# Kernel tuning notes

Hardware: AMD Instinct MI355X
Metric: run time of the kernel (lower is better)

The kernel has to match this reference:

```python
import jax, jax.numpy as jnp
import numpy as np

B, T, F, D = 4, 512, 512, 256


def setup_inputs() -> dict:
    key = jax.random.key(0)
    ks = jax.random.split(key, 7)
    x = jax.random.normal(ks[0], (B, T, F), jnp.float32)
    state = jnp.zeros((B, D, D), jnp.float32)
    init = lambda k, shape, fan: jax.random.normal(k, shape, jnp.float32) / np.sqrt(fan).astype(np.float32)
    Wk = init(ks[1], (F, D), F)
    Wq = init(ks[2], (F, D), F)
    Wv = init(ks[3], (F, D), F)
    Wbeta = init(ks[4], (F, 1), F)
    gamma = jnp.ones((F,), jnp.float32)
    beta_ln = jnp.zeros((F,), jnp.float32)
    Wsc = init(ks[5], (F, D), F)
    bsc = jnp.zeros((D,), jnp.float32)
    return dict(x=x, state=state, Wk=Wk, Wq=Wq, Wv=Wv, Wbeta=Wbeta,
                gamma=gamma, beta_ln=beta_ln, Wsc=Wsc, bsc=bsc)


def _layernorm(x, gamma, beta):
    mu = x.mean(-1, keepdims=True)
    var = x.var(-1, keepdims=True)  # ddof=0, matches torch LayerNorm
    return (x - mu) * jax.lax.rsqrt(var + 1e-5) * gamma + beta


def reference(x, state, Wk, Wq, Wv, Wbeta, gamma, beta_ln, Wsc, bsc):
    xn = _layernorm(x, gamma, beta_ln)                       # [B,T,F]
    K = jax.nn.relu(xn @ Wk)                                 # [B,T,D]
    Q = jax.nn.relu(xn @ Wq)                                 # [B,T,D]
    V = xn @ Wv                                              # [B,T,D]
    beta = jax.nn.sigmoid(xn @ Wbeta)                        # [B,T,1]
    # sum normalization
    K = K / (1e-5 + K.sum(-1, keepdims=True))
    Q = Q / (1e-5 + Q.sum(-1, keepdims=True))

    def step(s, inp):
        k, v, b = inp                                        # k,v:[B,D], b:[B,1]
        vbar = jnp.einsum('bij,bj->bi', s, k)                # retrieve
        s = s + (b * (v - vbar))[:, :, None] * k[:, None, :] # outer-product write
        return s, s

    Kt = jnp.moveaxis(K, 1, 0)  # [T,B,D]
    Vt = jnp.moveaxis(V, 1, 0)
    bt = jnp.moveaxis(beta, 1, 0)  # [T,B,1]
    _, states = jax.lax.scan(step, state, (Kt, Vt, bt))      # [T,B,D,D]
    states = jnp.moveaxis(states, 0, 1)                      # [B,T,D,D]

    y = jnp.einsum('btij,btj->bti', states, Q)               # [B,T,D]
    y = y + xn @ Wsc + bsc                                   # residual shortcut
    return y, states
```

## Files before the change

### kernel.cpp

```cpp
#include <hip/hip_runtime.h>
#include <math.h>

#define Bc 4
#define Tc 512
#define Fc 512
#define Dc 256
#define RPB 8
#define PF 4
#define CH 16
#define RS 4
#define NC (Tc / CH)

typedef float floatx4 __attribute__((ext_vector_type(4)));

__device__ __forceinline__ float wred(float v) {
#pragma unroll
  for (int off = 32; off; off >>= 1) v += __shfl_xor(v, off, 64);
  return v;
}

__device__ __forceinline__ float rl(float v, int l) {
  return __int_as_float(__builtin_amdgcn_readlane(__float_as_int(v), l));
}

__device__ __forceinline__ void wred2_dpp(float& a, float& c) {
#define DPP_STEP(ctrl, rmask)                                                 \
  {                                                                           \
    float ta = __int_as_float(__builtin_amdgcn_update_dpp(                    \
        0, __float_as_int(a), (ctrl), (rmask), 0xf, true));                   \
    float tc = __int_as_float(__builtin_amdgcn_update_dpp(                    \
        0, __float_as_int(c), (ctrl), (rmask), 0xf, true));                   \
    a += ta;                                                                  \
    c += tc;                                                                  \
  }
  DPP_STEP(0x111, 0xf)
  DPP_STEP(0x112, 0xf)
  DPP_STEP(0x114, 0xf)
  DPP_STEP(0x118, 0xf)
  DPP_STEP(0x142, 0xa)
  DPP_STEP(0x143, 0xc)
#undef DPP_STEP
  a = rl(a, 63);
  c = rl(c, 63);
}

__device__ __forceinline__ void ln_rows(const float* __restrict__ x,
                                        const float* __restrict__ gamma,
                                        const float* __restrict__ beta_ln,
                                        int row0, int wave, int lane,
                                        float (*xnL)[Fc]) {
#pragma unroll
  for (int rr = 0; rr < 2; ++rr) {
    const int r = wave * 2 + rr;
    const float* xr = x + (size_t)(row0 + r) * Fc;
    float4 a = *(const float4*)&xr[lane * 8];
    float4 b = *(const float4*)&xr[lane * 8 + 4];
    float s8 = a.x + a.y + a.z + a.w + b.x + b.y + b.z + b.w;
    float mu = wred(s8) * (1.0f / Fc);
    float d0 = a.x - mu, d1 = a.y - mu, d2 = a.z - mu, d3 = a.w - mu;
    float d4 = b.x - mu, d5 = b.y - mu, d6 = b.z - mu, d7 = b.w - mu;
    float sq = d0 * d0 + d1 * d1 + d2 * d2 + d3 * d3 + d4 * d4 + d5 * d5 +
               d6 * d6 + d7 * d7;
    float var = wred(sq) * (1.0f / Fc);
    float rs = rsqrtf(var + 1e-5f);
    float4 g0 = *(const float4*)&gamma[lane * 8];
    float4 g1 = *(const float4*)&gamma[lane * 8 + 4];
    float4 bl0 = *(const float4*)&beta_ln[lane * 8];
    float4 bl1 = *(const float4*)&beta_ln[lane * 8 + 4];
    float4 o0 = make_float4(d0 * rs * g0.x + bl0.x, d1 * rs * g0.y + bl0.y,
                            d2 * rs * g0.z + bl0.z, d3 * rs * g0.w + bl0.w);
    float4 o1 = make_float4(d4 * rs * g1.x + bl1.x, d5 * rs * g1.y + bl1.y,
                            d6 * rs * g1.z + bl1.z, d7 * rs * g1.w + bl1.w);
    *(float4*)&xnL[r][lane * 8] = o0;
    *(float4*)&xnL[r][lane * 8 + 4] = o1;
  }
}

__global__ __launch_bounds__(256, 2) void proj1_kernel(
    const float* __restrict__ x, const float* __restrict__ Wk,
    const float* __restrict__ Wq, const float* __restrict__ Wv,
    const float* __restrict__ gamma, const float* __restrict__ beta_ln,
    const float* __restrict__ Wsc, const float* __restrict__ bsc,
    float* __restrict__ Ko, float* __restrict__ Qo, float* __restrict__ Vo,
    float* __restrict__ ysco) {
  __shared__ __align__(16) float xn[RPB][Fc];

  const int tid = threadIdx.x;
  const int wave = tid >> 6, lane = tid & 63;
  const int bid = blockIdx.x;
  const int half = bid & 1;
  const int row0 = (bid >> 1) * RPB;
  const int col = half * 128 + (tid & 127);
  const int rg = tid >> 7;

  ln_rows(x, gamma, beta_ln, row0, wave, lane, xn);
  __syncthreads();

  float accK[4], accQ[4], accV[4], accS[4];
#pragma unroll
  for (int r = 0; r < 4; ++r) accK[r] = accQ[r] = accV[r] = accS[r] = 0.0f;

  for (int f = 0; f < Fc; f += 4) {
    float wk[4], wq[4], wv[4], ws[4];
#pragma unroll
    for (int ff = 0; ff < 4; ++ff) {
      wk[ff] = Wk[(size_t)(f + ff) * Dc + col];
      wq[ff] = Wq[(size_t)(f + ff) * Dc + col];
      wv[ff] = Wv[(size_t)(f + ff) * Dc + col];
      ws[ff] = Wsc[(size_t)(f + ff) * Dc + col];
    }
#pragma unroll
    for (int r = 0; r < 4; ++r) {
      float4 xr = *(const float4*)&xn[rg * 4 + r][f];
      accK[r] = fmaf(xr.w, wk[3], fmaf(xr.z, wk[2], fmaf(xr.y, wk[1], fmaf(xr.x, wk[0], accK[r]))));
      accQ[r] = fmaf(xr.w, wq[3], fmaf(xr.z, wq[2], fmaf(xr.y, wq[1], fmaf(xr.x, wq[0], accQ[r]))));
      accV[r] = fmaf(xr.w, wv[3], fmaf(xr.z, wv[2], fmaf(xr.y, wv[1], fmaf(xr.x, wv[0], accV[r]))));
      accS[r] = fmaf(xr.w, ws[3], fmaf(xr.z, ws[2], fmaf(xr.y, ws[1], fmaf(xr.x, ws[0], accS[r]))));
    }
  }

  const float bs = bsc[col];
#pragma unroll
  for (int r = 0; r < 4; ++r) {
    const size_t row = (size_t)(row0 + rg * 4 + r);
    Ko[row * Dc + col] = fmaxf(accK[r], 0.0f);
    Qo[row * Dc + col] = fmaxf(accQ[r], 0.0f);
    Vo[row * Dc + col] = accV[r];
    ysco[row * Dc + col] = accS[r] + bs;
  }
}

__global__ __launch_bounds__(256) void proj2_kernel(
    const float* __restrict__ x, const float* __restrict__ Wb,
    const float* __restrict__ gamma, const float* __restrict__ beta_ln,
    float* __restrict__ Ko, float* __restrict__ Qo, float* __restrict__ betao,
    float* __restrict__ kqo) {
  __shared__ __align__(16) float xn[RPB][Fc];
  __shared__ float red[4][32];
  __shared__ float fin[32];

  const int tid = threadIdx.x;
  const int wave = tid >> 6, lane = tid & 63;
  const int row0 = blockIdx.x * RPB;

  ln_rows(x, gamma, beta_ln, row0, wave, lane, xn);
  __syncthreads();

  const int d = tid;
  float pk[RPB], pq[RPB];
#pragma unroll
  for (int r = 0; r < RPB; ++r) {
    pk[r] = Ko[(size_t)(row0 + r) * Dc + d];
    pq[r] = Qo[(size_t)(row0 + r) * Dc + d];
  }
#pragma unroll
  for (int r = 0; r < RPB; ++r) {
    float p0 = wred(pk[r]);
    float p1 = wred(pq[r]);
    float p2 = wred(pk[r] * pq[r]);
    float pb = xn[r][tid] * Wb[tid] + xn[r][tid + 256] * Wb[tid + 256];
    float p3 = wred(pb);
    if (lane == 0) {
      red[wave][r * 4 + 0] = p0;
      red[wave][r * 4 + 1] = p1;
      red[wave][r * 4 + 2] = p2;
      red[wave][r * 4 + 3] = p3;
    }
  }
  __syncthreads();
  if (tid < 32) fin[tid] = red[0][tid] + red[1][tid] + red[2][tid] + red[3][tid];
  __syncthreads();

#pragma unroll
  for (int r = 0; r < RPB; ++r) {
    const size_t row = (size_t)(row0 + r);
    float invK = 1.0f / (1e-5f + fin[r * 4 + 0]);
    float invQ = 1.0f / (1e-5f + fin[r * 4 + 1]);
    Ko[row * Dc + d] = pk[r] * invK;
    Qo[row * Dc + d] = pq[r] * invQ;
  }
  if (tid < RPB) {
    const size_t row = (size_t)(row0 + tid);
    float invK = 1.0f / (1e-5f + fin[tid * 4 + 0]);
    float invQ = 1.0f / (1e-5f + fin[tid * 4 + 1]);
    betao[row] = 1.0f / (1.0f + expf(-fin[tid * 4 + 3]));
    kqo[row] = fin[tid * 4 + 2] * invK * invQ;
  }
}

__global__ __launch_bounds__(512) void scan_kernel(
    const float* __restrict__ S0, const float* __restrict__ K,
    const float* __restrict__ Q, const float* __restrict__ V,
    const float* __restrict__ ysc, const float* __restrict__ beta,
    const float* __restrict__ kq, float* __restrict__ yout,
    float* __restrict__ states) {
  __shared__ __align__(16) float ring_k[RS][CH][Dc];
  __shared__ float2 ring_uy[RS][CH][4];
  __shared__ int prog_a[4];
  __shared__ int prog_b[4];

  const int tid = threadIdx.x;
  const int wave = tid >> 6, lane = tid & 63;
  const int bid = blockIdx.x;
  const int xcd = bid & 7;
  const int slot = bid >> 3;
  const int b = xcd >> 1;
  const int sub = ((xcd & 1) << 5) | slot;
  const int i0 = sub * 4;

  if (tid < 4) {
    prog_a[tid] = 0;
    prog_b[tid] = 0;
  }
  __syncthreads();

  if (wave < 4) {
    const int i = i0 + wave;
    float4 s = *(const float4*)&S0[((size_t)(b * Dc + i)) * Dc + lane * 4];

    const float* Kb = K + (size_t)b * Tc * Dc;
    const float* Qb = Q + (size_t)b * Tc * Dc;
    const float* Vb = V + (size_t)b * Tc * Dc;
    const float* Yb = ysc + (size_t)b * Tc * Dc;
    const float* bb_p = beta + (size_t)b * Tc;
    const float* kq_p = kq + (size_t)b * Tc;

    float4 kb[PF], qb[PF];
#pragma unroll
    for (int j = 0; j < PF; ++j) {
      kb[j] = *(const float4*)&Kb[(size_t)j * Dc + lane * 4];
      qb[j] = *(const float4*)&Qb[(size_t)j * Dc + lane * 4];
    }
    const int sl = lane & 15;
    float vcur = Vb[(size_t)sl * Dc + i];
    float ycur = Yb[(size_t)sl * Dc + i];
    float bcur = bb_p[sl];
    float kqcur = kq_p[sl];

    for (int c = 0; c < NC; ++c) {
      if (c >= RS) {
        const int need = c - RS + 1;
#pragma unroll
        for (int m = 0; m < 4; ++m) {
          while (__hip_atomic_load(&prog_b[m], __ATOMIC_ACQUIRE,
                                   __HIP_MEMORY_SCOPE_WORKGROUP) < need)
            __builtin_amdgcn_s_sleep(2);
        }
      }
      const int cn = (c + 1 < NC) ? c + 1 : c;
      const int tbn = cn * CH;
      float vnxt = Vb[(size_t)(tbn + sl) * Dc + i];
      float ynxt = Yb[(size_t)(tbn + sl) * Dc + i];
      float bnxt = bb_p[tbn + sl];
      float kqnxt = kq_p[tbn + sl];

      const int r = c & (RS - 1);
      const int tb = c * CH;
#pragma unroll
      for (int j = 0; j < CH; ++j) {
        const int t = tb + j;
        const float4 k = kb[j & (PF - 1)];
        const float4 q = qb[j & (PF - 1)];
        const float vv = rl(vcur, j);
        const float yb = rl(ycur, j);
        const float bbs = rl(bcur, j);
        const float kqv = rl(kqcur, j);

        const int tn = (t + PF < Tc) ? t + PF : Tc - 1;
        kb[j & (PF - 1)] = *(const float4*)&Kb[(size_t)tn * Dc + lane * 4];
        qb[j & (PF - 1)] = *(const float4*)&Qb[(size_t)tn * Dc + lane * 4];

        float a = (s.x * k.x + s.y * k.y) + (s.z * k.z + s.w * k.w);
        float c2 = (s.x * q.x + s.y * q.y) + (s.z * q.z + s.w * q.w);
        wred2_dpp(a, c2);

        const float wcoef = bbs * (vv - a);
        s.x = fmaf(wcoef, k.x, s.x);
        s.y = fmaf(wcoef, k.y, s.y);
        s.z = fmaf(wcoef, k.z, s.z);
        s.w = fmaf(wcoef, k.w, s.w);

        if (wave == (j & 3)) *(float4*)&ring_k[r][j][lane * 4] = k;
        if (lane == 0) {
          float2 uy;
          uy.x = wcoef;
          uy.y = c2 + wcoef * kqv + yb;
          ring_uy[r][j][wave] = uy;
        }
      }
      __threadfence_block();
      __hip_atomic_store(&prog_a[wave], c + 1, __ATOMIC_RELEASE,
                         __HIP_MEMORY_SCOPE_WORKGROUP);
      vcur = vnxt;
      ycur = ynxt;
      bcur = bnxt;
      kqcur = kqnxt;
    }
  } else {
    const int wv = wave - 4;
    const int i = i0 + wv;
    float4 s = *(const float4*)&S0[((size_t)(b * Dc + i)) * Dc + lane * 4];

    for (int c = 0; c < NC; ++c) {
      const int need = c + 1;
#pragma unroll
      for (int m = 0; m < 4; ++m) {
        while (__hip_atomic_load(&prog_a[m], __ATOMIC_ACQUIRE,
                                 __HIP_MEMORY_SCOPE_WORKGROUP) < need)
          __builtin_amdgcn_s_sleep(2);
      }

      const int r = c & (RS - 1);
      const int tb = c * CH;
#pragma unroll
      for (int j = 0; j < CH; ++j) {
        const float2 uy = ring_uy[r][j][wv];
        const float4 k = *(const float4*)&ring_k[r][j][lane * 4];
        s.x = fmaf(uy.x, k.x, s.x);
        s.y = fmaf(uy.x, k.y, s.y);
        s.z = fmaf(uy.x, k.z, s.z);
        s.w = fmaf(uy.x, k.w, s.w);
        floatx4 sv;
        sv.x = s.x; sv.y = s.y; sv.z = s.z; sv.w = s.w;
        __builtin_nontemporal_store(
            sv, (floatx4*)&states[(((size_t)b * Tc + tb + j) * Dc + i) * Dc +
                                  lane * 4]);
        if (lane == 0) yout[((size_t)b * Tc + tb + j) * Dc + i] = uy.y;
      }
      __threadfence_block();
      __hip_atomic_store(&prog_b[wv], c + 1, __ATOMIC_RELEASE,
                         __HIP_MEMORY_SCOPE_WORKGROUP);
    }
  }
}

extern "C" void kernel_launch(void* const* d_in, const int* in_sizes, int n_in,
                              void* d_out, int out_size, void* d_ws,
                              size_t ws_size, hipStream_t stream) {
  const float* x = (const float*)d_in[0];
  const float* S0 = (const float*)d_in[1];
  const float* Wk = (const float*)d_in[2];
  const float* Wq = (const float*)d_in[3];
  const float* Wv = (const float*)d_in[4];
  const float* Wb = (const float*)d_in[5];
  const float* gamma = (const float*)d_in[6];
  const float* beta_ln = (const float*)d_in[7];
  const float* Wsc = (const float*)d_in[8];
  const float* bsc = (const float*)d_in[9];

  float* out = (float*)d_out;
  float* yout = out;
  float* states = out + (size_t)Bc * Tc * Dc;

  const size_t BTD = (size_t)Bc * Tc * Dc;
  float* ws = (float*)d_ws;
  float* K = ws;
  float* Q = K + BTD;
  float* V = Q + BTD;
  float* ysc = V + BTD;
  float* beta = ysc + BTD;
  float* kq = beta + (size_t)Bc * Tc;

  proj1_kernel<<<(Bc * Tc) / RPB * 2, 256, 0, stream>>>(
      x, Wk, Wq, Wv, gamma, beta_ln, Wsc, bsc, K, Q, V, ysc);
  proj2_kernel<<<(Bc * Tc) / RPB, 256, 0, stream>>>(x, Wb, gamma, beta_ln, K,
                                                    Q, beta, kq);
  scan_kernel<<<(Bc * Dc) / 4, 512, 0, stream>>>(S0, K, Q, V, ysc, beta, kq,
                                                 yout, states);
}
```

Baseline: 153.8 us.

## Split LayerNorm into own kernel and retile projection GEMM to 32x32 tiles

```diff
diff --git a/kernel.cpp b/kernel.cpp
--- a/kernel.cpp
+++ b/kernel.cpp
@@ -44,11 +44,12 @@
   c = rl(c, 63);
 }
 
-__device__ __forceinline__ void ln_rows(const float* __restrict__ x,
-                                        const float* __restrict__ gamma,
-                                        const float* __restrict__ beta_ln,
-                                        int row0, int wave, int lane,
-                                        float (*xnL)[Fc]) {
+__global__ __launch_bounds__(256) void ln_kernel(
+    const float* __restrict__ x, const float* __restrict__ gamma,
+    const float* __restrict__ beta_ln, float* __restrict__ xn_g) {
+  const int tid = threadIdx.x;
+  const int wave = tid >> 6, lane = tid & 63;
+  const int row0 = blockIdx.x * RPB;
 #pragma unroll
   for (int rr = 0; rr < 2; ++rr) {
     const int r = wave * 2 + rr;
@@ -67,55 +68,66 @@
     float4 g1 = *(const float4*)&gamma[lane * 8 + 4];
     float4 bl0 = *(const float4*)&beta_ln[lane * 8];
     float4 bl1 = *(const float4*)&beta_ln[lane * 8 + 4];
-    float4 o0 = make_float4(d0 * rs * g0.x + bl0.x, d1 * rs * g0.y + bl0.y,
-                            d2 * rs * g0.z + bl0.z, d3 * rs * g0.w + bl0.w);
-    float4 o1 = make_float4(d4 * rs * g1.x + bl1.x, d5 * rs * g1.y + bl1.y,
-                            d6 * rs * g1.z + bl1.z, d7 * rs * g1.w + bl1.w);
-    *(float4*)&xnL[r][lane * 8] = o0;
-    *(float4*)&xnL[r][lane * 8 + 4] = o1;
+    float* xo = xn_g + (size_t)(row0 + r) * Fc;
+    *(float4*)&xo[lane * 8] =
+        make_float4(d0 * rs * g0.x + bl0.x, d1 * rs * g0.y + bl0.y,
+                    d2 * rs * g0.z + bl0.z, d3 * rs * g0.w + bl0.w);
+    *(float4*)&xo[lane * 8 + 4] =
+        make_float4(d4 * rs * g1.x + bl1.x, d5 * rs * g1.y + bl1.y,
+                    d6 * rs * g1.z + bl1.z, d7 * rs * g1.w + bl1.w);
   }
 }
 
 __global__ __launch_bounds__(256, 2) void proj1_kernel(
-    const float* __restrict__ x, const float* __restrict__ Wk,
+    const float* __restrict__ xn_g, const float* __restrict__ Wk,
     const float* __restrict__ Wq, const float* __restrict__ Wv,
-    const float* __restrict__ gamma, const float* __restrict__ beta_ln,
     const float* __restrict__ Wsc, const float* __restrict__ bsc,
     float* __restrict__ Ko, float* __restrict__ Qo, float* __restrict__ Vo,
     float* __restrict__ ysco) {
-  __shared__ __align__(16) float xn[RPB][Fc];
+  __shared__ __align__(16) float xs[32][128];
 
   const int tid = threadIdx.x;
-  const int wave = tid >> 6, lane = tid & 63;
   const int bid = blockIdx.x;
-  const int half = bid & 1;
-  const int row0 = (bid >> 1) * RPB;
-  const int col = half * 128 + (tid & 127);
-  const int rg = tid >> 7;
-
-  ln_rows(x, gamma, beta_ln, row0, wave, lane, xn);
-  __syncthreads();
+  const int ct = bid & 7;
+  const int rt = bid >> 3;
+  const int row0 = rt * 32;
+  const int col = ct * 32 + (tid & 31);
+  const int rg = tid >> 5;
 
   float accK[4], accQ[4], accV[4], accS[4];
 #pragma unroll
   for (int r = 0; r < 4; ++r) accK[r] = accQ[r] = accV[r] = accS[r] = 0.0f;
 
-  for (int f = 0; f < Fc; f += 4) {
-    float wk[4], wq[4], wv[4], ws[4];
-#pragma unroll
-    for (int ff = 0; ff < 4; ++ff) {
-      wk[ff] = Wk[(size_t)(f + ff) * Dc + col];
-      wq[ff] = Wq[(size_t)(f + ff) * Dc + col];
-      wv[ff] = Wv[(size_t)(f + ff) * Dc + col];
-      ws[ff] = Wsc[(size_t)(f + ff) * Dc + col];
-    }
-#pragma unroll
-    for (int r = 0; r < 4; ++r) {
-      float4 xr = *(const float4*)&xn[rg * 4 + r][f];
-      accK[r] = fmaf(xr.w, wk[3], fmaf(xr.z, wk[2], fmaf(xr.y, wk[1], fmaf(xr.x, wk[0], accK[r]))));
-      accQ[r] = fmaf(xr.w, wq[3], fmaf(xr.z, wq[2], fmaf(xr.y, wq[1], fmaf(xr.x, wq[0], accQ[r]))));
-      accV[r] = fmaf(xr.w, wv[3], fmaf(xr.z, wv[2], fmaf(xr.y, wv[1], fmaf(xr.x, wv[0], accV[r]))));
-      accS[r] = fmaf(xr.w, ws[3], fmaf(xr.z, ws[2], fmaf(xr.y, ws[1], fmaf(xr.x, ws[0], accS[r]))));
+  for (int fc = 0; fc < Fc; fc += 128) {
+    __syncthreads();
+#pragma unroll
+    for (int m = 0; m < 4; ++m) {
+      const int e = tid + 256 * m;
+      const int r = e >> 5;
+      const int c4 = e & 31;
+      *(float4*)&xs[r][c4 * 4] =
+          *(const float4*)&xn_g[(size_t)(row0 + r) * Fc + fc + c4 * 4];
+    }
+    __syncthreads();
+
+    for (int f4 = 0; f4 < 128; f4 += 4) {
+      float wk[4], wq[4], wv[4], ws[4];
+#pragma unroll
+      for (int ff = 0; ff < 4; ++ff) {
+        const size_t off = (size_t)(fc + f4 + ff) * Dc + col;
+        wk[ff] = Wk[off];
+        wq[ff] = Wq[off];
+        wv[ff] = Wv[off];
+        ws[ff] = Wsc[off];
+      }
+#pragma unroll
+      for (int r = 0; r < 4; ++r) {
+        float4 xr = *(const float4*)&xs[rg * 4 + r][f4];
+        accK[r] = fmaf(xr.w, wk[3], fmaf(xr.z, wk[2], fmaf(xr.y, wk[1], fmaf(xr.x, wk[0], accK[r]))));
+        accQ[r] = fmaf(xr.w, wq[3], fmaf(xr.z, wq[2], fmaf(xr.y, wq[1], fmaf(xr.x, wq[0], accQ[r]))));
+        accV[r] = fmaf(xr.w, wv[3], fmaf(xr.z, wv[2], fmaf(xr.y, wv[1], fmaf(xr.x, wv[0], accV[r]))));
+        accS[r] = fmaf(xr.w, ws[3], fmaf(xr.z, ws[2], fmaf(xr.y, ws[1], fmaf(xr.x, ws[0], accS[r]))));
+      }
     }
   }
 
@@ -131,8 +143,7 @@
 }
 
 __global__ __launch_bounds__(256) void proj2_kernel(
-    const float* __restrict__ x, const float* __restrict__ Wb,
-    const float* __restrict__ gamma, const float* __restrict__ beta_ln,
+    const float* __restrict__ xn_g, const float* __restrict__ Wb,
     float* __restrict__ Ko, float* __restrict__ Qo, float* __restrict__ betao,
     float* __restrict__ kqo) {
   __shared__ __align__(16) float xn[RPB][Fc];
@@ -143,7 +154,14 @@
   const int wave = tid >> 6, lane = tid & 63;
   const int row0 = blockIdx.x * RPB;
 
-  ln_rows(x, gamma, beta_ln, row0, wave, lane, xn);
+#pragma unroll
+  for (int m = 0; m < 4; ++m) {
+    const int e = tid + 256 * m;
+    const int r = e >> 7;
+    const int c4 = e & 127;
+    *(float4*)&xn[r][c4 * 4] =
+        *(const float4*)&xn_g[(size_t)(row0 + r) * Fc + c4 * 4];
+  }
   __syncthreads();
 
   const int d = tid;
@@ -361,10 +379,12 @@
   float* beta = ysc + BTD;
   float* kq = beta + (size_t)Bc * Tc;
 
-  proj1_kernel<<<(Bc * Tc) / RPB * 2, 256, 0, stream>>>(
-      x, Wk, Wq, Wv, gamma, beta_ln, Wsc, bsc, K, Q, V, ysc);
-  proj2_kernel<<<(Bc * Tc) / RPB, 256, 0, stream>>>(x, Wb, gamma, beta_ln, K,
-                                                    Q, beta, kq);
+  float* xn_g = states;
+
+  ln_kernel<<<(Bc * Tc) / RPB, 256, 0, stream>>>(x, gamma, beta_ln, xn_g);
+  proj1_kernel<<<512, 256, 0, stream>>>(xn_g, Wk, Wq, Wv, Wsc, bsc, K, Q, V,
+                                        ysc);
+  proj2_kernel<<<(Bc * Tc) / RPB, 256, 0, stream>>>(xn_g, Wb, K, Q, beta, kq);
   scan_kernel<<<(Bc * Dc) / 4, 512, 0, stream>>>(S0, K, Q, V, ysc, beta, kq,
                                                  yout, states);
 }
```

Result: slower. 222.2 us (+44.5%).
